# Kernel tuning notes

Hardware: AMD Instinct MI355X
Metric: run time of the kernel (lower is better)

The kernel has to match this reference:

```python
import jax, jax.numpy as jnp
import numpy as np

S = 3        # message passing steps
L = 128      # latent size
N = 10000    # nodes
E = 160000   # edges
DN, DE, DG = 64, 16, 8
OUT = 8
EPS = 1e-5


def _ln(x, scale, offset):
    m = jnp.mean(x, axis=-1, keepdims=True)
    v = jnp.var(x, axis=-1, keepdims=True)
    return (x - m) * jax.lax.rsqrt(v + EPS) * scale + offset


def _mlp(x, W0, b0, W1, b1):
    h = jax.nn.relu(x @ W0 + b0)
    return jax.nn.relu(h @ W1 + b1)


def setup_inputs() -> dict:
    key = jax.random.key(0)
    ks = iter(jax.random.split(key, 64))

    def w(shape, fan_in):
        return jax.random.normal(next(ks), shape, jnp.float32) / np.sqrt(fan_in).astype(np.float32)

    inp = {
        "nodes": jax.random.normal(next(ks), (N, DN), jnp.float32),
        "edges": jax.random.normal(next(ks), (E, DE), jnp.float32),
        "globals_": jax.random.normal(next(ks), (1, DG), jnp.float32),
        "senders": jax.random.randint(next(ks), (E,), 0, N),
        "receivers": jax.random.randint(next(ks), (E,), 0, N),
        # embedder
        "emb_node_W": w((DN, L), DN), "emb_node_b": jnp.zeros((L,), jnp.float32),
        "emb_edge_W": w((DE, L), DE), "emb_edge_b": jnp.zeros((L,), jnp.float32),
        "emb_glob_W": w((DG, L), DG), "emb_glob_b": jnp.zeros((L,), jnp.float32),
        # per-step MLPs (2 layers each)
        "edge_W0": w((S, 4 * L, L), 4 * L), "edge_b0": jnp.zeros((S, L), jnp.float32),
        "edge_W1": w((S, L, L), L),         "edge_b1": jnp.zeros((S, L), jnp.float32),
        "node_W0": w((S, 4 * L, L), 4 * L), "node_b0": jnp.zeros((S, L), jnp.float32),
        "node_W1": w((S, L, L), L),         "node_b1": jnp.zeros((S, L), jnp.float32),
        "glob_W0": w((S, 3 * L, L), 3 * L), "glob_b0": jnp.zeros((S, L), jnp.float32),
        "glob_W1": w((S, L, L), L),         "glob_b1": jnp.zeros((S, L), jnp.float32),
        # per-step layernorm (0: nodes, 1: edges, 2: globals)
        "ln_scale": jnp.ones((S, 3, L), jnp.float32),
        "ln_offset": jnp.zeros((S, 3, L), jnp.float32),
        # decoder (globals only)
        "dec_W": w((L, OUT), L), "dec_b": jnp.zeros((OUT,), jnp.float32),
    }
    return inp


def reference(nodes, edges, globals_, senders, receivers,
              emb_node_W, emb_node_b, emb_edge_W, emb_edge_b, emb_glob_W, emb_glob_b,
              edge_W0, edge_b0, edge_W1, edge_b1,
              node_W0, node_b0, node_W1, node_b1,
              glob_W0, glob_b0, glob_W1, glob_b1,
              ln_scale, ln_offset, dec_W, dec_b):
    # embed to latent
    n = nodes @ emb_node_W + emb_node_b      # [N, L]
    e = edges @ emb_edge_W + emb_edge_b      # [E, L]
    g = globals_ @ emb_glob_W + emb_glob_b   # [1, L]

    for s in range(S):
        # edge update: concat(edges, nodes[senders], nodes[receivers], globals)
        g_e = jnp.broadcast_to(g, (e.shape[0], L))
        e_in = jnp.concatenate([e, n[senders], n[receivers], g_e], axis=-1)  # [E, 4L]
        e_new = _mlp(e_in, edge_W0[s], edge_b0[s], edge_W1[s], edge_b1[s])
        # node update: concat(nodes, segsum(e,senders), segsum(e,receivers), globals)
        sent_agg = jax.ops.segment_sum(e_new, senders, num_segments=N)
        recv_agg = jax.ops.segment_sum(e_new, receivers, num_segments=N)
        g_n = jnp.broadcast_to(g, (N, L))
        n_in = jnp.concatenate([n, sent_agg, recv_agg, g_n], axis=-1)  # [N, 4L]
        n_new = _mlp(n_in, node_W0[s], node_b0[s], node_W1[s], node_b1[s])
        # global update: concat(node_agg, edge_agg, globals) (single graph)
        node_agg = jnp.sum(n_new, axis=0, keepdims=True)
        edge_agg = jnp.sum(e_new, axis=0, keepdims=True)
        g_in = jnp.concatenate([node_agg, edge_agg, g], axis=-1)  # [1, 3L]
        g_new = _mlp(g_in, glob_W0[s], glob_b0[s], glob_W1[s], glob_b1[s])
        # residual + layernorm
        n = _ln(n_new + n, ln_scale[s, 0], ln_offset[s, 0])
        e = _ln(e_new + e, ln_scale[s, 1], ln_offset[s, 1])
        g = _ln(g_new + g, ln_scale[s, 2], ln_offset[s, 2])

    # decoder maps globals only
    return g @ dec_W + dec_b  # [1, OUT]
```

## Files before the change

kernel.cpp:

```cpp
#include <hip/hip_runtime.h>
#include <hip/hip_bf16.h>

typedef __bf16 bf16;
typedef __bf16 bf16x8 __attribute__((ext_vector_type(8)));
typedef __bf16 bf16x4 __attribute__((ext_vector_type(4)));
typedef float  f32x4  __attribute__((ext_vector_type(4)));

#define NL 128
#define NN 10000
#define NE 160000
#define LN_EPS 1e-5f

__device__ __forceinline__ f32x4 f4zero() {
    f32x4 v; v[0] = 0.f; v[1] = 0.f; v[2] = 0.f; v[3] = 0.f; return v;
}

__device__ __forceinline__ int swz_off(int row, int b) {
    return row * 256 + (b ^ ((row & 7) << 4));
}

__device__ __forceinline__ bf16x8 frag_ld(const bf16* base, int row, int kbyte) {
    return *reinterpret_cast<const bf16x8*>(
        reinterpret_cast<const char*>(base) + swz_off(row, kbyte));
}

template <int NT>
__device__ __forceinline__ void stage_img(const bf16* __restrict__ img, bf16* dst, int tid) {
    #pragma unroll
    for (int i = 0; i < 2048 / NT; ++i) {
        int byte = (i * NT + tid) * 16;
        *reinterpret_cast<bf16x8*>(reinterpret_cast<char*>(dst) + byte) =
            *reinterpret_cast<const bf16x8*>(reinterpret_cast<const char*>(img) + byte);
    }
}

template <int NT>
__device__ __forceinline__ void stage_img_ld(const bf16* __restrict__ img, bf16x8* r, int tid) {
    #pragma unroll
    for (int i = 0; i < 2048 / NT; ++i)
        r[i] = *reinterpret_cast<const bf16x8*>(reinterpret_cast<const char*>(img) +
                                                (i * NT + tid) * 16);
}
template <int NT>
__device__ __forceinline__ void stage_img_st(bf16* dst, const bf16x8* r, int tid) {
    #pragma unroll
    for (int i = 0; i < 2048 / NT; ++i)
        *reinterpret_cast<bf16x8*>(reinterpret_cast<char*>(dst) + (i * NT + tid) * 16) = r[i];
}

__device__ __forceinline__ void stage_rows16(const float* __restrict__ src0, bf16* sX,
                                             int wrow0, int lane) {
    int c8 = (lane & 15) * 8;
    #pragma unroll
    for (int i = 0; i < 4; ++i) {
        int sub = i * 4 + (lane >> 4);
        const float* src = src0 + (size_t)sub * 128 + c8;
        f32x4 a = *reinterpret_cast<const f32x4*>(src);
        f32x4 b = *reinterpret_cast<const f32x4*>(src + 4);
        bf16x8 v;
        v[0] = (bf16)a[0]; v[1] = (bf16)a[1]; v[2] = (bf16)a[2]; v[3] = (bf16)a[3];
        v[4] = (bf16)b[0]; v[5] = (bf16)b[1]; v[6] = (bf16)b[2]; v[7] = (bf16)b[3];
        *reinterpret_cast<bf16x8*>(reinterpret_cast<char*>(sX) + swz_off(wrow0 + sub, c8 * 2)) = v;
    }
}

__device__ __forceinline__ void mfma_16x128(const bf16* sA, const bf16* sB, int arow, int kq,
                                            f32x4 acc[8]) {
    #pragma unroll
    for (int kk = 0; kk < 4; ++kk) {
        bf16x8 af = frag_ld(sA, arow, kk * 64 + kq);
        #pragma unroll
        for (int t = 0; t < 8; ++t) {
            bf16x8 bfr = frag_ld(sB, t * 16 + (arow & 15), kk * 64 + kq);
            acc[t] = __builtin_amdgcn_mfma_f32_16x16x32_bf16(af, bfr, acc[t], 0, 0, 0);
        }
    }
}

__device__ __forceinline__ void acc_to_lds_bf16(bf16* sX, const f32x4 acc[8], int w, int lane) {
    int c0 = lane & 15;
    #pragma unroll
    for (int r = 0; r < 4; ++r) {
        int rl = w * 16 + (lane >> 4) * 4 + r;
        #pragma unroll
        for (int t = 0; t < 8; ++t) {
            int col = t * 16 + c0;
            *reinterpret_cast<bf16*>(reinterpret_cast<char*>(sX) + swz_off(rl, col * 2)) =
                (bf16)acc[t][r];
        }
    }
}

__device__ __forceinline__ void lds_rows_to_global_bf16(const bf16* sX, bf16* __restrict__ dst0,
                                                        int w, int lane) {
    int c8 = (lane & 15) * 8;
    #pragma unroll
    for (int i = 0; i < 4; ++i) {
        int sub = i * 4 + (lane >> 4);
        bf16x8 v = *reinterpret_cast<const bf16x8*>(
            reinterpret_cast<const char*>(sX) + swz_off(w * 16 + sub, c8 * 2));
        *reinterpret_cast<bf16x8*>(dst0 + (size_t)sub * 128 + c8) = v;
    }
}

__global__ void k_prep(const float* __restrict__ eW0, const float* __restrict__ eW1,
                       const float* __restrict__ nW0, const float* __restrict__ nW1,
                       bf16* __restrict__ imgs, const float* __restrict__ globals_,
                       const float* __restrict__ embW, const float* __restrict__ embB,
                       float* __restrict__ g, const float* __restrict__ eb0,
                       const float* __restrict__ nb0, float* __restrict__ gve,
                       float* __restrict__ gvn, int* __restrict__ deg,
                       float* __restrict__ eagg, float* __restrict__ nagg,
                       int* __restrict__ done) {
    const int b = blockIdx.x;
    const int tid = threadIdx.x;
    if (b < 24) {
        const int s = b >> 3, kind = b & 7;
        const float* src;
        if (kind < 3)       src = eW0 + (size_t)s * 512 * 128 + (size_t)kind * 128 * 128;
        else if (kind == 3) src = eW1 + (size_t)s * 128 * 128;
        else if (kind < 7)  src = nW0 + (size_t)s * 512 * 128 + (size_t)(kind - 4) * 128 * 128;
        else                src = nW1 + (size_t)s * 128 * 128;
        bf16* img = imgs + (size_t)b * 16384;
        for (int i = 0; i < 16; ++i) {
            int q = tid + i * 256;
            int col = q & 127;
            int k0 = (q >> 7) << 2;
            bf16x4 v;
            v[0] = (bf16)src[(k0 + 0) * 128 + col];
            v[1] = (bf16)src[(k0 + 1) * 128 + col];
            v[2] = (bf16)src[(k0 + 2) * 128 + col];
            v[3] = (bf16)src[(k0 + 3) * 128 + col];
            *reinterpret_cast<bf16x4*>(reinterpret_cast<char*>(img) + swz_off(col, k0 * 2)) = v;
        }
    } else if (b == 24) {
        __shared__ float sG[128];
        if (tid < 3) done[tid] = 0;
        if (tid < 128) {
            float a = embB[tid];
            #pragma unroll
            for (int k = 0; k < 8; ++k) a += globals_[k] * embW[k * 128 + tid];
            g[tid] = a;
            sG[tid] = a;
        }
        __syncthreads();
        if (tid < 128) {
            const float* eW0g = eW0 + 384 * 128;
            const float* nW0g = nW0 + 384 * 128;
            float ae = eb0[tid], an = nb0[tid];
            for (int k = 0; k < 128; ++k) {
                float gv = sG[k];
                ae += gv * eW0g[k * 128 + tid];
                an += gv * nW0g[k * 128 + tid];
            }
            gve[tid] = ae;
            gvn[tid] = an;
        }
    } else {
        for (int i = tid; i < 2 * NN; i += 256) deg[i] = 0;
        for (int i = tid; i < 8 * 128; i += 256) eagg[i] = 0.f;
        for (int i = tid; i < 4 * 128; i += 256) nagg[i] = 0.f;
    }
}


__global__ void k_hist(const int* __restrict__ senders, const int* __restrict__ receivers,
                       int* __restrict__ deg_s, int* __restrict__ deg_r) {
    int i = blockIdx.x * 256 + threadIdx.x;
    if (i < NE) {
        atomicAdd(&deg_s[senders[i]], 1);
        atomicAdd(&deg_r[receivers[i]], 1);
    }
}

__device__ void scan_arr(const int* __restrict__ deg, int* __restrict__ rs, int* __restrict__ cur,
                         int* sW, int* sRun) {
    const int tid = threadIdx.x, lane = tid & 63, wid = tid >> 6;
    if (tid == 0) *sRun = 0;
    __syncthreads();
    for (int base = 0; base < NN; base += 1024) {
        int i = base + tid;
        int orig = (i < NN) ? deg[i] : 0;
        int v = orig;
        #pragma unroll
        for (int off = 1; off < 64; off <<= 1) {
            int u = __shfl_up(v, off, 64);
            if (lane >= off) v += u;
        }
        if (lane == 63) sW[wid] = v;
        __syncthreads();
        if (wid == 0 && lane < 16) {
            int u = sW[lane];
            #pragma unroll
            for (int off = 1; off < 16; off <<= 1) {
                int t = __shfl_up(u, off, 16);
                if (lane >= off) u += t;
            }
            sW[lane] = u;
        }
        __syncthreads();
        int waveoff = (wid == 0) ? 0 : sW[wid - 1];
        int incl = v + waveoff + *sRun;
        if (i < NN) {
            rs[i + 1] = incl;
            cur[i] = incl - orig;
        }
        __syncthreads();
        if (tid == 1023) *sRun = incl;
        __syncthreads();
    }
    if (tid == 0) rs[0] = 0;
}

__global__ void k_scan(const int* __restrict__ deg_s, int* __restrict__ rs_s,
                       int* __restrict__ cur_s, const int* __restrict__ deg_r,
                       int* __restrict__ rs_r, int* __restrict__ cur_r) {
    __shared__ int sW[16];
    __shared__ int sRun;
    scan_arr(deg_s, rs_s, cur_s, sW, &sRun);
    __syncthreads();
    scan_arr(deg_r, rs_r, cur_r, sW, &sRun);
}

__global__ void k_scatter_s(const int* __restrict__ senders, const int* __restrict__ receivers,
                            int* __restrict__ cur_s, int* __restrict__ perm,
                            int* __restrict__ snd_s, int* __restrict__ rcv_s) {
    int i = blockIdx.x * 256 + threadIdx.x;
    if (i < NE) {
        int s = senders[i];
        int p = atomicAdd(&cur_s[s], 1);
        perm[p] = i;
        snd_s[p] = s;
        rcv_s[p] = receivers[i];
    }
}

__global__ void k_scatter_r(const int* __restrict__ rcv_s, int* __restrict__ cur_r,
                            int* __restrict__ csr_r) {
    int j = blockIdx.x * 256 + threadIdx.x;
    if (j < NE) {
        int r = rcv_s[j];
        int p = atomicAdd(&cur_r[r], 1);
        csr_r[p] = j;
    }
}


__global__ __launch_bounds__(256, 2) void k_embed_nodes(
    const float* __restrict__ nodes, const float* __restrict__ W, const float* __restrict__ b,
    float* __restrict__ n_out, const bf16* __restrict__ imgPs, const bf16* __restrict__ imgPr,
    bf16* __restrict__ nsW, bf16* __restrict__ nrW) {
    __shared__ __align__(16) char smem[81920];
    float* sWemb = (float*)smem;
    float* sB = (float*)(smem + 32768);
    bf16* sWa = (bf16*)smem;
    bf16* sWb = (bf16*)(smem + 32768);
    bf16* sX = (bf16*)(smem + 65536);
    const int tid = threadIdx.x;
    const int lane = tid & 63;
    const int w = tid >> 6;
    const int rowbase = blockIdx.x * 64;
    const bool wvalid = (rowbase + w * 16) < NN;

    for (int i = tid; i < 64 * 128; i += 256) sWemb[i] = W[i];
    if (tid < 128) sB[tid] = b[tid];
    __syncthreads();

    const int rg = tid >> 4;
    const int c8 = (tid & 15) * 8;
    #pragma unroll
    for (int p = 0; p < 4; ++p) {
        int row = rowbase + p * 16 + rg;
        if (row < NN) {
            const f32x4* x4 = reinterpret_cast<const f32x4*>(nodes + (size_t)row * 64);
            float o[8];
            #pragma unroll
            for (int j = 0; j < 8; ++j) o[j] = sB[c8 + j];
            #pragma unroll
            for (int k4 = 0; k4 < 16; ++k4) {
                f32x4 xv = x4[k4];
                #pragma unroll
                for (int kk = 0; kk < 4; ++kk) {
                    float x = xv[kk];
                    const float* wrow = sWemb + (k4 * 4 + kk) * 128 + c8;
                    f32x4 wA = *reinterpret_cast<const f32x4*>(wrow);
                    f32x4 wB = *reinterpret_cast<const f32x4*>(wrow + 4);
                    o[0] += x * wA[0]; o[1] += x * wA[1]; o[2] += x * wA[2]; o[3] += x * wA[3];
                    o[4] += x * wB[0]; o[5] += x * wB[1]; o[6] += x * wB[2]; o[7] += x * wB[3];
                }
            }
            f32x4 oA, oB;
            bf16x8 v;
            #pragma unroll
            for (int j = 0; j < 8; ++j) {
                if (j < 4) oA[j] = o[j]; else oB[j - 4] = o[j];
                v[j] = (bf16)o[j];
            }
            float* orow = n_out + (size_t)row * 128 + c8;
            *reinterpret_cast<f32x4*>(orow) = oA;
            *reinterpret_cast<f32x4*>(orow + 4) = oB;
            *reinterpret_cast<bf16x8*>(reinterpret_cast<char*>(sX) +
                                       swz_off(p * 16 + rg, c8 * 2)) = v;
        }
    }
    __syncthreads();
    stage_img<256>(imgPs, sWa, tid);
    stage_img<256>(imgPr, sWb, tid);
    __syncthreads();
    if (!wvalid) return;

    const int arow = w * 16 + (lane & 15);
    const int kq = (lane >> 4) * 16;
    f32x4 acc[8], acc2[8];
    #pragma unroll
    for (int t = 0; t < 8; ++t) { acc[t] = f4zero(); acc2[t] = f4zero(); }
    mfma_16x128(sX, sWa, arow, kq, acc);
    mfma_16x128(sX, sWb, arow, kq, acc2);

    acc_to_lds_bf16(sX, acc, w, lane);
    lds_rows_to_global_bf16(sX, nsW + (size_t)(rowbase + w * 16) * 128, w, lane);
    acc_to_lds_bf16(sX, acc2, w, lane);
    lds_rows_to_global_bf16(sX, nrW + (size_t)(rowbase + w * 16) * 128, w, lane);
}

__global__ __launch_bounds__(256) void k_embed_edges(const float* __restrict__ edges,
                                                     const int* __restrict__ perm,
                                                     const float* __restrict__ W,
                                                     const float* __restrict__ b,
                                                     bf16* __restrict__ e_out) {
    __shared__ float sW[16 * 128];
    __shared__ float sB[128];
    const int tid = threadIdx.x;
    for (int i = tid; i < 16 * 128; i += 256) sW[i] = W[i];
    if (tid < 128) sB[tid] = b[tid];
    __syncthreads();
    const int rg = tid >> 4;
    const int c8 = (tid & 15) * 8;
    const int rowbase = blockIdx.x * 128;
    #pragma unroll 2
    for (int p = 0; p < 8; ++p) {
        int row = rowbase + p * 16 + rg;
        int src = perm[row];
        const f32x4* x4 = reinterpret_cast<const f32x4*>(edges + (size_t)src * 16);
        f32x4 xr0 = x4[0], xr1 = x4[1], xr2 = x4[2], xr3 = x4[3];
        float o[8];
        #pragma unroll
        for (int j = 0; j < 8; ++j) o[j] = sB[c8 + j];
        f32x4 xr[4] = {xr0, xr1, xr2, xr3};
        #pragma unroll
        for (int q = 0; q < 4; ++q) {
            #pragma unroll
            for (int kk = 0; kk < 4; ++kk) {
                float x = xr[q][kk];
                const float* wrow = sW + (q * 4 + kk) * 128 + c8;
                f32x4 wA = *reinterpret_cast<const f32x4*>(wrow);
                f32x4 wB = *reinterpret_cast<const f32x4*>(wrow + 4);
                o[0] += x * wA[0]; o[1] += x * wA[1]; o[2] += x * wA[2]; o[3] += x * wA[3];
                o[4] += x * wB[0]; o[5] += x * wB[1]; o[6] += x * wB[2]; o[7] += x * wB[3];
            }
        }
        bf16x8 v;
        #pragma unroll
        for (int j = 0; j < 8; ++j) v[j] = (bf16)o[j];
        *reinterpret_cast<bf16x8*>(e_out + (size_t)row * 128 + c8) = v;
    }
}


__global__ __launch_bounds__(512, 2) void k_edge(
    bf16* e_rw, bf16* __restrict__ e_new_out, const bf16* __restrict__ nsW,
    const bf16* __restrict__ nrW, float* __restrict__ edge_agg,
    const int* __restrict__ snd_s, const int* __restrict__ rcv_s,
    const bf16* __restrict__ imgW0, const bf16* __restrict__ imgW1,
    const float* __restrict__ gvec, const float* __restrict__ b1,
    const float* __restrict__ lnS, const float* __restrict__ lnO) {
    __shared__ __align__(16) char smem[65536];
    bf16* sW = (bf16*)smem;
    bf16* sX = (bf16*)(smem + 32768);
    float* sEagg = (float*)smem;

    const int tid = threadIdx.x;
    const int lane = tid & 63;
    const int w = tid >> 6;
    const int rowbase = blockIdx.x * 128;
    const int arow = w * 16 + (lane & 15);
    const int kq = (lane >> 4) * 16;
    const int c0 = lane & 15;
    const int qrt = lane >> 4;
    const int c8 = c0 * 8;

    stage_img<512>(imgW0, sW, tid);

    int snd_i[4], rcv_i[4];
    bf16x8 eold8[4];
    #pragma unroll
    for (int i = 0; i < 4; ++i) {
        int gr = rowbase + w * 16 + i * 4 + qrt;
        snd_i[i] = snd_s[gr];
        rcv_i[i] = rcv_s[gr];
        eold8[i] = *reinterpret_cast<const bf16x8*>(e_rw + (size_t)gr * 128 + c8);
    }

    f32x4 gvA = *reinterpret_cast<const f32x4*>(gvec + c8);
    f32x4 gvB = *reinterpret_cast<const f32x4*>(gvec + c8 + 4);
    f32x4 lsA = *reinterpret_cast<const f32x4*>(lnS + c8);
    f32x4 lsB = *reinterpret_cast<const f32x4*>(lnS + c8 + 4);
    f32x4 loA = *reinterpret_cast<const f32x4*>(lnO + c8);
    f32x4 loB = *reinterpret_cast<const f32x4*>(lnO + c8 + 4);
    float bb[8];
    #pragma unroll
    for (int t = 0; t < 8; ++t) bb[t] = b1[t * 16 + c0];

    bf16x8 ns8[4], nr8[4];
    #pragma unroll
    for (int i = 0; i < 4; ++i) {
        ns8[i] = *reinterpret_cast<const bf16x8*>(nsW + (size_t)snd_i[i] * 128 + c8);
        nr8[i] = *reinterpret_cast<const bf16x8*>(nrW + (size_t)rcv_i[i] * 128 + c8);
    }

    #pragma unroll
    for (int i = 0; i < 4; ++i)
        *reinterpret_cast<bf16x8*>(reinterpret_cast<char*>(sX) +
                                   swz_off(w * 16 + i * 4 + qrt, c8 * 2)) = eold8[i];

    __syncthreads();

    f32x4 acc[8];
    #pragma unroll
    for (int t = 0; t < 8; ++t) acc[t] = f4zero();
    __builtin_amdgcn_s_setprio(1);
    mfma_16x128(sX, sW, arow, kq, acc);
    __builtin_amdgcn_s_setprio(0);

    __syncthreads();

    bf16x8 w1r[4];
    stage_img_ld<512>(imgW1, w1r, tid);

    #pragma unroll
    for (int r = 0; r < 4; ++r) {
        int rl = w * 16 + (lane >> 4) * 4 + r;
        #pragma unroll
        for (int t = 0; t < 8; ++t)
            *reinterpret_cast<bf16*>(reinterpret_cast<char*>(sX) +
                                     swz_off(rl, (t * 16 + c0) * 2)) = (bf16)acc[t][r];
    }
    #pragma unroll
    for (int i = 0; i < 4; ++i) {
        int rl = w * 16 + i * 4 + qrt;
        bf16x8 a8 = *reinterpret_cast<const bf16x8*>(
            reinterpret_cast<const char*>(sX) + swz_off(rl, c8 * 2));
        bf16x8 h8;
        #pragma unroll
        for (int j = 0; j < 8; ++j) {
            float gvj = (j < 4) ? gvA[j] : gvB[j - 4];
            float v = (float)a8[j] + (float)ns8[i][j] + (float)nr8[i][j] + gvj;
            h8[j] = (bf16)fmaxf(v, 0.f);
        }
        *reinterpret_cast<bf16x8*>(reinterpret_cast<char*>(sX) + swz_off(rl, c8 * 2)) = h8;
    }

    stage_img_st<512>(sW, w1r, tid);
    __syncthreads();

    f32x4 acc2[8];
    #pragma unroll
    for (int t = 0; t < 8; ++t) acc2[t] = f4zero();
    __builtin_amdgcn_s_setprio(1);
    mfma_16x128(sX, sW, arow, kq, acc2);
    __builtin_amdgcn_s_setprio(0);

    #pragma unroll
    for (int r = 0; r < 4; ++r) {
        int rl = w * 16 + (lane >> 4) * 4 + r;
        #pragma unroll
        for (int t = 0; t < 8; ++t)
            *reinterpret_cast<bf16*>(reinterpret_cast<char*>(sX) +
                                     swz_off(rl, (t * 16 + c0) * 2)) =
                (bf16)fmaxf(acc2[t][r] + bb[t], 0.f);
    }

    float cs[8];
    #pragma unroll
    for (int j = 0; j < 8; ++j) cs[j] = 0.f;
    bf16* enew0 = e_new_out + (size_t)rowbase * 128;
    bf16* e0 = e_rw + (size_t)rowbase * 128;
    #pragma unroll
    for (int i = 0; i < 4; ++i) {
        int sub = w * 16 + i * 4 + qrt;
        bf16x8 en8 = *reinterpret_cast<const bf16x8*>(
            reinterpret_cast<const char*>(sX) + swz_off(sub, c8 * 2));
        *reinterpret_cast<bf16x8*>(enew0 + (size_t)sub * 128 + c8) = en8;
        float rv[8], s1 = 0.f, s2 = 0.f;
        #pragma unroll
        for (int j = 0; j < 8; ++j) {
            float en = (float)en8[j];
            cs[j] += en;
            float v = en + (float)eold8[i][j];
            rv[j] = v;
            s1 += v;
            s2 += v * v;
        }
        #pragma unroll
        for (int off = 1; off < 16; off <<= 1) {
            s1 += __shfl_xor(s1, off, 16);
            s2 += __shfl_xor(s2, off, 16);
        }
        float mean = s1 * (1.f / 128.f);
        float rstd = rsqrtf(s2 * (1.f / 128.f) - mean * mean + LN_EPS);
        bf16x8 o8;
        #pragma unroll
        for (int j = 0; j < 8; ++j) {
            float ls = (j < 4) ? lsA[j] : lsB[j - 4];
            float lo = (j < 4) ? loA[j] : loB[j - 4];
            o8[j] = (bf16)((rv[j] - mean) * rstd * ls + lo);
        }
        *reinterpret_cast<bf16x8*>(e0 + (size_t)sub * 128 + c8) = o8;
    }

    #pragma unroll
    for (int j = 0; j < 8; ++j) {
        cs[j] += __shfl_xor(cs[j], 16, 64);
        cs[j] += __shfl_xor(cs[j], 32, 64);
    }
    __syncthreads();
    if (qrt == 0) {
        float* dst = sEagg + w * 128 + c8;
        #pragma unroll
        for (int j = 0; j < 8; ++j) dst[j] = cs[j];
    }
    __syncthreads();
    if (tid < 128) {
        float v = 0.f;
        #pragma unroll
        for (int ww = 0; ww < 8; ++ww) v += sEagg[ww * 128 + tid];
        atomicAdd(&edge_agg[(blockIdx.x & 7) * 128 + tid], v);
    }
}

__global__ __launch_bounds__(256) void k_agg(const bf16* __restrict__ e_new,
                                             const int* __restrict__ rs_s,
                                             const int* __restrict__ rs_r,
                                             const int* __restrict__ csr_r,
                                             bf16* __restrict__ sent, bf16* __restrict__ recv) {
    const int lane = threadIdx.x & 63;
    const int w = threadIdx.x >> 6;
    const int node = blockIdx.x * 4 + w;
    if (node >= NN) return;
    const int qrt = lane >> 4;
    const int c8 = (lane & 15) * 8;
    float a[8];
    #pragma unroll
    for (int j = 0; j < 8; ++j) a[j] = 0.f;
    const int b0 = rs_s[node], b1 = rs_s[node + 1];
    for (int jj = b0 + qrt; jj < b1; jj += 4) {
        bf16x8 v = *reinterpret_cast<const bf16x8*>(e_new + (size_t)jj * 128 + c8);
        #pragma unroll
        for (int j = 0; j < 8; ++j) a[j] += (float)v[j];
    }
    #pragma unroll
    for (int j = 0; j < 8; ++j) {
        a[j] += __shfl_xor(a[j], 16, 64);
        a[j] += __shfl_xor(a[j], 32, 64);
    }
    if (qrt == 0) {
        bf16x8 o;
        #pragma unroll
        for (int j = 0; j < 8; ++j) o[j] = (bf16)a[j];
        *reinterpret_cast<bf16x8*>(sent + (size_t)node * 128 + c8) = o;
    }
    #pragma unroll
    for (int j = 0; j < 8; ++j) a[j] = 0.f;
    const int c1 = rs_r[node], c2 = rs_r[node + 1];
    for (int pp = c1 + qrt; pp < c2; pp += 4) {
        int jj = csr_r[pp];
        bf16x8 v = *reinterpret_cast<const bf16x8*>(e_new + (size_t)jj * 128 + c8);
        #pragma unroll
        for (int j = 0; j < 8; ++j) a[j] += (float)v[j];
    }
    #pragma unroll
    for (int j = 0; j < 8; ++j) {
        a[j] += __shfl_xor(a[j], 16, 64);
        a[j] += __shfl_xor(a[j], 32, 64);
    }
    if (qrt == 0) {
        bf16x8 o;
        #pragma unroll
        for (int j = 0; j < 8; ++j) o[j] = (bf16)a[j];
        *reinterpret_cast<bf16x8*>(recv + (size_t)node * 128 + c8) = o;
    }
}

__global__ __launch_bounds__(256, 2) void k_node(
    float* n_rw, const bf16* __restrict__ sent, const bf16* __restrict__ recv,
    float* __restrict__ node_agg , const bf16* __restrict__ imgW0,
    const bf16* __restrict__ imgW1, const float* __restrict__ gvec,
    const float* __restrict__ b1, const float* __restrict__ lnS,
    const float* __restrict__ lnO, const bf16* __restrict__ imgPs,
    const bf16* __restrict__ imgPr, bf16* __restrict__ nsW, bf16* __restrict__ nrW,
    int do_proj,
    int* __restrict__ done_ctr, float* __restrict__ edge_agg , float* __restrict__ g,
    const float* __restrict__ gW0, const float* __restrict__ gb0,
    const float* __restrict__ gW1, const float* __restrict__ gb1,
    const float* __restrict__ glnS, const float* __restrict__ glnO,
    const float* __restrict__ eW0g, const float* __restrict__ eb0n,
    const float* __restrict__ nW0g, const float* __restrict__ nb0n,
    float* __restrict__ gve, float* __restrict__ gvn, const float* __restrict__ decW,
    const float* __restrict__ decb, float* __restrict__ out, int do_next, int do_dec) {
    __shared__ __align__(16) char smem[81920];
    __shared__ int sLast;
    bf16* sA = (bf16*)smem;
    bf16* sB = (bf16*)(smem + 32768);
    bf16* sX = (bf16*)(smem + 65536);
    float* sNagg = (float*)smem;

    const int tid = threadIdx.x;
    const int lane = tid & 63;
    const int w = tid >> 6;
    const int rowbase = blockIdx.x * 64;
    const bool wvalid = (rowbase + w * 16) < NN;
    const int arow = w * 16 + (lane & 15);
    const int kq = (lane >> 4) * 16;
    const int c0 = lane & 15;
    const int qrt = lane >> 4;
    const int c8 = c0 * 8;

    stage_img<256>(imgW0, sA, tid);
    stage_img<256>(imgW0 + 16384, sB, tid);
    bf16x8 sent8[4], recv8[4];
    if (wvalid) {
        stage_rows16(n_rw + (size_t)(rowbase + w * 16) * 128, sX, w * 16, lane);
        #pragma unroll
        for (int i = 0; i < 4; ++i) {
            int gr = rowbase + w * 16 + i * 4 + qrt;
            sent8[i] = *reinterpret_cast<const bf16x8*>(sent + (size_t)gr * 128 + c8);
            recv8[i] = *reinterpret_cast<const bf16x8*>(recv + (size_t)gr * 128 + c8);
        }
    }
    __syncthreads();

    float gvf[8], bbf[8];
    #pragma unroll
    for (int t = 0; t < 8; ++t) {
        gvf[t] = gvec[t * 16 + c0];
        bbf[t] = b1[t * 16 + c0];
    }
    f32x4 lsA4 = *reinterpret_cast<const f32x4*>(lnS + c8);
    f32x4 lsB4 = *reinterpret_cast<const f32x4*>(lnS + c8 + 4);
    f32x4 loA4 = *reinterpret_cast<const f32x4*>(lnO + c8);
    f32x4 loB4 = *reinterpret_cast<const f32x4*>(lnO + c8 + 4);

    f32x4 acc[8];
    #pragma unroll
    for (int t = 0; t < 8; ++t) acc[t] = f4zero();
    float cs[8];
    #pragma unroll
    for (int j = 0; j < 8; ++j) cs[j] = 0.f;

    if (wvalid) mfma_16x128(sX, sA, arow, kq, acc);
    __syncthreads();

    stage_img<256>(imgW0 + 32768, sA, tid);
    if (wvalid) {
        #pragma unroll
        for (int i = 0; i < 4; ++i)
            *reinterpret_cast<bf16x8*>(reinterpret_cast<char*>(sX) +
                                       swz_off(w * 16 + i * 4 + qrt, c8 * 2)) = sent8[i];
        mfma_16x128(sX, sB, arow, kq, acc);
    }
    __syncthreads();

    stage_img<256>(imgW1, sB, tid);
    if (wvalid) {
        #pragma unroll
        for (int i = 0; i < 4; ++i)
            *reinterpret_cast<bf16x8*>(reinterpret_cast<char*>(sX) +
                                       swz_off(w * 16 + i * 4 + qrt, c8 * 2)) = recv8[i];
        mfma_16x128(sX, sA, arow, kq, acc);

        #pragma unroll
        for (int r = 0; r < 4; ++r) {
            int rl = w * 16 + (lane >> 4) * 4 + r;
            #pragma unroll
            for (int t = 0; t < 8; ++t)
                *reinterpret_cast<bf16*>(reinterpret_cast<char*>(sX) +
                                         swz_off(rl, (t * 16 + c0) * 2)) =
                    (bf16)fmaxf(acc[t][r] + gvf[t], 0.f);
        }
    }
    __syncthreads();

    if (wvalid) {
        #pragma unroll
        for (int t = 0; t < 8; ++t) acc[t] = f4zero();
        mfma_16x128(sX, sB, arow, kq, acc);
        #pragma unroll
        for (int r = 0; r < 4; ++r) {
            int rl = w * 16 + (lane >> 4) * 4 + r;
            #pragma unroll
            for (int t = 0; t < 8; ++t)
                *reinterpret_cast<bf16*>(reinterpret_cast<char*>(sX) +
                                         swz_off(rl, (t * 16 + c0) * 2)) =
                    (bf16)fmaxf(acc[t][r] + bbf[t], 0.f);
        }

        const float* nbase = n_rw + (size_t)(rowbase + w * 16) * 128;
        #pragma unroll
        for (int i = 0; i < 4; ++i) {
            int sub = i * 4 + qrt;
            bf16x8 en8 = *reinterpret_cast<const bf16x8*>(
                reinterpret_cast<const char*>(sX) + swz_off(w * 16 + sub, c8 * 2));
            f32x4 noA = *reinterpret_cast<const f32x4*>(nbase + (size_t)sub * 128 + c8);
            f32x4 noB = *reinterpret_cast<const f32x4*>(nbase + (size_t)sub * 128 + c8 + 4);
            float rv[8], s1 = 0.f, s2 = 0.f;
            #pragma unroll
            for (int j = 0; j < 8; ++j) {
                float en = (float)en8[j];
                cs[j] += en;
                float v = en + ((j < 4) ? noA[j] : noB[j - 4]);
                rv[j] = v;
                s1 += v;
                s2 += v * v;
            }
            #pragma unroll
            for (int off = 1; off < 16; off <<= 1) {
                s1 += __shfl_xor(s1, off, 16);
                s2 += __shfl_xor(s2, off, 16);
            }
            float mean = s1 * (1.f / 128.f);
            float rstd = rsqrtf(s2 * (1.f / 128.f) - mean * mean + LN_EPS);
            f32x4 oA, oB;
            bf16x8 l8;
            #pragma unroll
            for (int j = 0; j < 8; ++j) {
                float ls = (j < 4) ? lsA4[j] : lsB4[j - 4];
                float lo = (j < 4) ? loA4[j] : loB4[j - 4];
                float o = (rv[j] - mean) * rstd * ls + lo;
                if (j < 4) oA[j] = o; else oB[j - 4] = o;
                l8[j] = (bf16)o;
            }
            float* orow = n_rw + (size_t)(rowbase + w * 16 + sub) * 128 + c8;
            *reinterpret_cast<f32x4*>(orow) = oA;
            *reinterpret_cast<f32x4*>(orow + 4) = oB;
            *reinterpret_cast<bf16x8*>(reinterpret_cast<char*>(sX) +
                                       swz_off(w * 16 + sub, c8 * 2)) = l8;
        }
    }

    if (do_proj) {
        __syncthreads();
        stage_img<256>(imgPs, sA, tid);
        stage_img<256>(imgPr, sB, tid);
        __syncthreads();
        if (wvalid) {
            f32x4 pa[8], pb[8];
            #pragma unroll
            for (int t = 0; t < 8; ++t) { pa[t] = f4zero(); pb[t] = f4zero(); }
            mfma_16x128(sX, sA, arow, kq, pa);
            mfma_16x128(sX, sB, arow, kq, pb);
            acc_to_lds_bf16(sX, pa, w, lane);
            lds_rows_to_global_bf16(sX, nsW + (size_t)(rowbase + w * 16) * 128, w, lane);
            acc_to_lds_bf16(sX, pb, w, lane);
            lds_rows_to_global_bf16(sX, nrW + (size_t)(rowbase + w * 16) * 128, w, lane);
        }
    }

    #pragma unroll
    for (int j = 0; j < 8; ++j) {
        cs[j] += __shfl_xor(cs[j], 16, 64);
        cs[j] += __shfl_xor(cs[j], 32, 64);
    }
    __syncthreads();
    if (qrt == 0) {
        float* dst = sNagg + w * 128 + c8;
        #pragma unroll
        for (int j = 0; j < 8; ++j) dst[j] = wvalid ? cs[j] : 0.f;
    }
    __syncthreads();
    if (tid < 128) {
        float v = sNagg[tid] + sNagg[128 + tid] + sNagg[256 + tid] + sNagg[384 + tid];
        atomicAdd(&node_agg[(blockIdx.x & 3) * 128 + tid], v);
    }

    __syncthreads();
    if (tid == 0) {
        __threadfence();
        int old = atomicAdd(done_ctr, 1);
        sLast = (old == (int)gridDim.x - 1);
    }
    __syncthreads();
    if (!sLast) return;

    float* sIn = (float*)smem;
    float* sP0 = sIn + 384;
    float* sP1 = sP0 + 128;
    float* sH = sP1 + 128;
    float* sG = sH + 128;
    float* sMR = sG + 128;
    const int j = tid & 127;
    const int part = tid >> 7;

    if (tid < 128) {
        float v = 0.f;
        #pragma unroll
        for (int c = 0; c < 4; ++c) v += atomicAdd(&node_agg[c * 128 + tid], 0.f);
        #pragma unroll
        for (int c = 0; c < 4; ++c) atomicExch(&node_agg[c * 128 + tid], 0.f);
        sIn[tid] = v;
        sIn[256 + tid] = g[tid];
    } else {
        float v = 0.f;
        #pragma unroll
        for (int c = 0; c < 8; ++c) v += edge_agg[c * 128 + j];
        #pragma unroll
        for (int c = 0; c < 8; ++c) edge_agg[c * 128 + j] = 0.f;
        sIn[128 + j] = v;
    }
    __syncthreads();
    {
        float p = 0.f;
        for (int k = 0; k < 192; ++k) {
            int kk = part * 192 + k;
            p += sIn[kk] * gW0[(size_t)kk * 128 + j];
        }
        (part ? sP1 : sP0)[j] = p;
    }
    __syncthreads();
    if (tid < 128) sH[tid] = fmaxf(gb0[tid] + sP0[tid] + sP1[tid], 0.f);
    __syncthreads();
    {
        float p = 0.f;
        for (int k = 0; k < 64; ++k) {
            int kk = part * 64 + k;
            p += sH[kk] * gW1[(size_t)kk * 128 + j];
        }
        (part ? sP1 : sP0)[j] = p;
    }
    __syncthreads();
    float res = 0.f;
    if (tid < 128) {
        res = fmaxf(gb1[tid] + sP0[tid] + sP1[tid], 0.f) + sIn[256 + tid];
        sP0[tid] = res;
        sP1[tid] = res * res;
    }
    __syncthreads();
    if (tid < 64) {
        float a = sP0[tid] + sP0[tid + 64];
        float q = sP1[tid] + sP1[tid + 64];
        #pragma unroll
        for (int off = 1; off < 64; off <<= 1) {
            a += __shfl_xor(a, off, 64);
            q += __shfl_xor(q, off, 64);
        }
        if (tid == 0) {
            float m = a * (1.f / 128.f);
            float v = q * (1.f / 128.f) - m * m;
            sMR[0] = m;
            sMR[1] = rsqrtf(v + LN_EPS);
        }
    }
    __syncthreads();
    if (tid < 128) {
        float go = (res - sMR[0]) * sMR[1] * glnS[tid] + glnO[tid];
        g[tid] = go;
        sG[tid] = go;
    }
    __syncthreads();
    if (do_next) {
        float pe = 0.f, pn = 0.f;
        for (int k = 0; k < 64; ++k) {
            int kk = part * 64 + k;
            float gv = sG[kk];
            pe += gv * eW0g[(size_t)kk * 128 + j];
            pn += gv * nW0g[(size_t)kk * 128 + j];
        }
        (part ? sP1 : sP0)[j] = pe;
        sIn[part * 128 + j] = pn;
        __syncthreads();
        if (tid < 128) {
            gve[tid] = eb0n[tid] + sP0[tid] + sP1[tid];
            gvn[tid] = nb0n[tid] + sIn[tid] + sIn[128 + tid];
        }
    }
    if (do_dec && tid < 8) {
        float a = decb[tid];
        for (int k = 0; k < 128; ++k) a += sG[k] * decW[k * 8 + tid];
        out[tid] = a;
    }
}

extern "C" void kernel_launch(void* const* d_in, const int* in_sizes, int n_in, void* d_out,
                              int out_size, void* d_ws, size_t ws_size, hipStream_t stream) {
    (void)in_sizes; (void)n_in; (void)out_size; (void)ws_size;
    const float* nodes = (const float*)d_in[0];
    const float* edges = (const float*)d_in[1];
    const float* globals_ = (const float*)d_in[2];
    const int* senders = (const int*)d_in[3];
    const int* receivers = (const int*)d_in[4];
    const float* emb_node_W = (const float*)d_in[5];
    const float* emb_node_b = (const float*)d_in[6];
    const float* emb_edge_W = (const float*)d_in[7];
    const float* emb_edge_b = (const float*)d_in[8];
    const float* emb_glob_W = (const float*)d_in[9];
    const float* emb_glob_b = (const float*)d_in[10];
    const float* edge_W0 = (const float*)d_in[11];
    const float* edge_b0 = (const float*)d_in[12];
    const float* edge_W1 = (const float*)d_in[13];
    const float* edge_b1 = (const float*)d_in[14];
    const float* node_W0 = (const float*)d_in[15];
    const float* node_b0 = (const float*)d_in[16];
    const float* node_W1 = (const float*)d_in[17];
    const float* node_b1 = (const float*)d_in[18];
    const float* glob_W0 = (const float*)d_in[19];
    const float* glob_b0 = (const float*)d_in[20];
    const float* glob_W1 = (const float*)d_in[21];
    const float* glob_b1 = (const float*)d_in[22];
    const float* ln_scale = (const float*)d_in[23];
    const float* ln_offset = (const float*)d_in[24];
    const float* dec_W = (const float*)d_in[25];
    const float* dec_b = (const float*)d_in[26];

    char* ws = (char*)d_ws;
    size_t off = 0;
    auto alloc = [&](size_t bytes) -> char* {
        char* p = ws + off;
        off += (bytes + 255) & ~(size_t)255;
        return p;
    };
    bf16* e = (bf16*)alloc((size_t)NE * NL * 2);
    bf16* e_new = (bf16*)alloc((size_t)NE * NL * 2);
    float* n = (float*)alloc((size_t)NN * NL * 4);
    bf16* nsW = (bf16*)alloc((size_t)NN * NL * 2);
    bf16* nrW = (bf16*)alloc((size_t)NN * NL * 2);
    bf16* sent = (bf16*)alloc((size_t)NN * NL * 2);
    bf16* recv = (bf16*)alloc((size_t)NN * NL * 2);
    bf16* imgs = (bf16*)alloc((size_t)24 * 16384 * 2);
    float* eagg = (float*)alloc(8 * 128 * 4);
    float* nagg = (float*)alloc(4 * 128 * 4);
    float* g = (float*)alloc(128 * 4);
    float* gve = (float*)alloc(128 * 4);
    float* gvn = (float*)alloc(128 * 4);
    int* done = (int*)alloc(16 * 4);
    int* deg = (int*)alloc((size_t)2 * NN * 4);
    int* deg_s = deg;
    int* deg_r = deg + NN;
    int* rs_s = (int*)alloc((size_t)(NN + 1) * 4);
    int* rs_r = (int*)alloc((size_t)(NN + 1) * 4);
    int* cur_s = (int*)alloc((size_t)NN * 4);
    int* cur_r = (int*)alloc((size_t)NN * 4);
    int* perm = (int*)alloc((size_t)NE * 4);
    int* snd_s = (int*)alloc((size_t)NE * 4);
    int* rcv_s = (int*)alloc((size_t)NE * 4);
    int* csr_r = (int*)alloc((size_t)NE * 4);

    const int NB_N = (NN + 63) / 64;
    const int NB_E = NE / 128;
    const int NB_EMB = NE / 128;
    const int NB_SC = (NE + 255) / 256;
    const int NB_AGG = NN / 4;

    auto img = [&](int s, int kind) -> const bf16* {
        return imgs + ((size_t)s * 8 + kind) * 16384;
    };

    k_prep<<<26, 256, 0, stream>>>(edge_W0, edge_W1, node_W0, node_W1, imgs, globals_,
                                   emb_glob_W, emb_glob_b, g, edge_b0, node_b0, gve, gvn,
                                   deg, eagg, nagg, done);

    k_hist<<<NB_SC, 256, 0, stream>>>(senders, receivers, deg_s, deg_r);
    k_scan<<<1, 1024, 0, stream>>>(deg_s, rs_s, cur_s, deg_r, rs_r, cur_r);
    k_scatter_s<<<NB_SC, 256, 0, stream>>>(senders, receivers, cur_s, perm, snd_s, rcv_s);
    k_scatter_r<<<NB_SC, 256, 0, stream>>>(rcv_s, cur_r, csr_r);

    k_embed_nodes<<<NB_N, 256, 0, stream>>>(nodes, emb_node_W, emb_node_b, n, img(0, 1),
                                            img(0, 2), nsW, nrW);
    k_embed_edges<<<NB_EMB, 256, 0, stream>>>(edges, perm, emb_edge_W, emb_edge_b, e);

    for (int s = 0; s < 3; ++s) {
        const int last = (s == 2);
        k_edge<<<NB_E, 512, 0, stream>>>(e, e_new, nsW, nrW, eagg, snd_s, rcv_s, img(s, 0),
                                         img(s, 3), gve, edge_b1 + s * 128,
                                         ln_scale + (s * 3 + 1) * 128,
                                         ln_offset + (s * 3 + 1) * 128);
        k_agg<<<NB_AGG, 256, 0, stream>>>(e_new, rs_s, rs_r, csr_r, sent, recv);
        const float* eW0g = last ? edge_W0 : edge_W0 + (size_t)(s + 1) * 512 * 128 + 384 * 128;
        const float* eb0n = last ? edge_b0 : edge_b0 + (s + 1) * 128;
        const float* nW0g = last ? node_W0 : node_W0 + (size_t)(s + 1) * 512 * 128 + 384 * 128;
        const float* nb0n = last ? node_b0 : node_b0 + (s + 1) * 128;
        k_node<<<NB_N, 256, 0, stream>>>(
            n, sent, recv, nagg, img(s, 4), img(s, 7), gvn, node_b1 + s * 128,
            ln_scale + (s * 3 + 0) * 128, ln_offset + (s * 3 + 0) * 128,
            img(last ? 0 : s + 1, 1), img(last ? 0 : s + 1, 2), nsW, nrW, !last,
            done + s, eagg, g, glob_W0 + (size_t)s * 384 * 128, glob_b0 + s * 128,
            glob_W1 + (size_t)s * 128 * 128, glob_b1 + s * 128, ln_scale + (s * 3 + 2) * 128,
            ln_offset + (s * 3 + 2) * 128, eW0g, eb0n, nW0g, nb0n, gve, gvn, dec_W, dec_b,
            (float*)d_out, !last, last);
    }
}
```

Measured before the change: 401.0 us.

## Read MFMA weight fragments from global, fuse sender aggregation into edge kernel

Weight images are pre-laid out in per-lane MFMA fragment order so the GEMMs load B fragments straight from global or L2 instead of staging them into LDS. Shared memory drops sharply and most block barriers go away, and the edge kernel now runs 64-row, 256-thread blocks to raise occupancy. Sender-side segment sums move into the edge kernel as run-length fp32 atomics, using the fact that edges are sorted by sender. The fp32 sent buffer is zeroed in the prep kernel and re-zeroed by the node kernel after it is read. This trades LDS reuse for repeated global fragment reads and adds atomic traffic.

```diff
diff --git a/kernel.cpp b/kernel.cpp
--- a/kernel.cpp
+++ b/kernel.cpp
@@ -3,11 +3,11 @@
 
 typedef __bf16 bf16;
 typedef __bf16 bf16x8 __attribute__((ext_vector_type(8)));
-typedef __bf16 bf16x4 __attribute__((ext_vector_type(4)));
 typedef float  f32x4  __attribute__((ext_vector_type(4)));
 
 #define NL 128
 #define NN 10000
+#define NNPAD 10048
 #define NE 160000
 #define LN_EPS 1e-5f
 
@@ -22,30 +22,6 @@
 __device__ __forceinline__ bf16x8 frag_ld(const bf16* base, int row, int kbyte) {
     return *reinterpret_cast<const bf16x8*>(
         reinterpret_cast<const char*>(base) + swz_off(row, kbyte));
-}
-
-template <int NT>
-__device__ __forceinline__ void stage_img(const bf16* __restrict__ img, bf16* dst, int tid) {
-    #pragma unroll
-    for (int i = 0; i < 2048 / NT; ++i) {
-        int byte = (i * NT + tid) * 16;
-        *reinterpret_cast<bf16x8*>(reinterpret_cast<char*>(dst) + byte) =
-            *reinterpret_cast<const bf16x8*>(reinterpret_cast<const char*>(img) + byte);
-    }
-}
-
-template <int NT>
-__device__ __forceinline__ void stage_img_ld(const bf16* __restrict__ img, bf16x8* r, int tid) {
-    #pragma unroll
-    for (int i = 0; i < 2048 / NT; ++i)
-        r[i] = *reinterpret_cast<const bf16x8*>(reinterpret_cast<const char*>(img) +
-                                                (i * NT + tid) * 16);
-}
-template <int NT>
-__device__ __forceinline__ void stage_img_st(bf16* dst, const bf16x8* r, int tid) {
-    #pragma unroll
-    for (int i = 0; i < 2048 / NT; ++i)
-        *reinterpret_cast<bf16x8*>(reinterpret_cast<char*>(dst) + (i * NT + tid) * 16) = r[i];
 }
 
 __device__ __forceinline__ void stage_rows16(const float* __restrict__ src0, bf16* sX,
@@ -64,14 +40,15 @@
     }
 }
 
-__device__ __forceinline__ void mfma_16x128(const bf16* sA, const bf16* sB, int arow, int kq,
-                                            f32x4 acc[8]) {
+__device__ __forceinline__ void mfma_16x128g(const bf16* sA, const bf16* __restrict__ imgB,
+                                             int arow, int kq, int lane, f32x4 acc[8]) {
     #pragma unroll
     for (int kk = 0; kk < 4; ++kk) {
         bf16x8 af = frag_ld(sA, arow, kk * 64 + kq);
         #pragma unroll
         for (int t = 0; t < 8; ++t) {
-            bf16x8 bfr = frag_ld(sB, t * 16 + (arow & 15), kk * 64 + kq);
+            bf16x8 bfr = *reinterpret_cast<const bf16x8*>(
+                imgB + (size_t)(((kk * 8 + t) * 64 + lane)) * 8);
             acc[t] = __builtin_amdgcn_mfma_f32_16x16x32_bf16(af, bfr, acc[t], 0, 0, 0);
         }
     }
@@ -111,7 +88,7 @@
                        const float* __restrict__ nb0, float* __restrict__ gve,
                        float* __restrict__ gvn, int* __restrict__ deg,
                        float* __restrict__ eagg, float* __restrict__ nagg,
-                       int* __restrict__ done) {
+                       float* __restrict__ sent, int* __restrict__ done) {
     const int b = blockIdx.x;
     const int tid = threadIdx.x;
     if (b < 24) {
@@ -122,16 +99,18 @@
         else if (kind < 7)  src = nW0 + (size_t)s * 512 * 128 + (size_t)(kind - 4) * 128 * 128;
         else                src = nW1 + (size_t)s * 128 * 128;
         bf16* img = imgs + (size_t)b * 16384;
-        for (int i = 0; i < 16; ++i) {
+        #pragma unroll
+        for (int i = 0; i < 8; ++i) {
             int q = tid + i * 256;
-            int col = q & 127;
-            int k0 = (q >> 7) << 2;
-            bf16x4 v;
-            v[0] = (bf16)src[(k0 + 0) * 128 + col];
-            v[1] = (bf16)src[(k0 + 1) * 128 + col];
-            v[2] = (bf16)src[(k0 + 2) * 128 + col];
-            v[3] = (bf16)src[(k0 + 3) * 128 + col];
-            *reinterpret_cast<bf16x4*>(reinterpret_cast<char*>(img) + swz_off(col, k0 * 2)) = v;
+            int l = q & 63;
+            int ft = q >> 6;
+            int kk = ft >> 3, t = ft & 7;
+            int col = t * 16 + (l & 15);
+            int k0 = kk * 32 + (l >> 4) * 8;
+            bf16x8 v;
+            #pragma unroll
+            for (int j = 0; j < 8; ++j) v[j] = (bf16)src[(size_t)(k0 + j) * 128 + col];
+            *reinterpret_cast<bf16x8*>(img + (size_t)q * 8) = v;
         }
     } else if (b == 24) {
         __shared__ float sG[128];
@@ -156,10 +135,17 @@
             gve[tid] = ae;
             gvn[tid] = an;
         }
-    } else {
+    } else if (b == 25) {
         for (int i = tid; i < 2 * NN; i += 256) deg[i] = 0;
         for (int i = tid; i < 8 * 128; i += 256) eagg[i] = 0.f;
         for (int i = tid; i < 4 * 128; i += 256) nagg[i] = 0.f;
+    } else {
+        const int chunk = NNPAD * 128 / 16;
+        float* base = sent + (size_t)(b - 26) * chunk;
+        for (int i = tid * 4; i < chunk; i += 1024) {
+            f32x4 z = f4zero();
+            *reinterpret_cast<f32x4*>(base + i) = z;
+        }
     }
 }
 
@@ -250,12 +236,10 @@
     const float* __restrict__ nodes, const float* __restrict__ W, const float* __restrict__ b,
     float* __restrict__ n_out, const bf16* __restrict__ imgPs, const bf16* __restrict__ imgPr,
     bf16* __restrict__ nsW, bf16* __restrict__ nrW) {
-    __shared__ __align__(16) char smem[81920];
+    __shared__ __align__(16) char smem[49664];
     float* sWemb = (float*)smem;
     float* sB = (float*)(smem + 32768);
-    bf16* sWa = (bf16*)smem;
-    bf16* sWb = (bf16*)(smem + 32768);
-    bf16* sX = (bf16*)(smem + 65536);
+    bf16* sX = (bf16*)(smem + 33280);
     const int tid = threadIdx.x;
     const int lane = tid & 63;
     const int w = tid >> 6;
@@ -267,7 +251,7 @@
     __syncthreads();
 
     const int rg = tid >> 4;
-    const int c8 = (tid & 15) * 8;
+    const int c8e = (tid & 15) * 8;
     #pragma unroll
     for (int p = 0; p < 4; ++p) {
         int row = rowbase + p * 16 + rg;
@@ -275,14 +259,14 @@
             const f32x4* x4 = reinterpret_cast<const f32x4*>(nodes + (size_t)row * 64);
             float o[8];
             #pragma unroll
-            for (int j = 0; j < 8; ++j) o[j] = sB[c8 + j];
+            for (int j = 0; j < 8; ++j) o[j] = sB[c8e + j];
             #pragma unroll
             for (int k4 = 0; k4 < 16; ++k4) {
                 f32x4 xv = x4[k4];
                 #pragma unroll
                 for (int kk = 0; kk < 4; ++kk) {
                     float x = xv[kk];
-                    const float* wrow = sWemb + (k4 * 4 + kk) * 128 + c8;
+                    const float* wrow = sWemb + (k4 * 4 + kk) * 128 + c8e;
                     f32x4 wA = *reinterpret_cast<const f32x4*>(wrow);
                     f32x4 wB = *reinterpret_cast<const f32x4*>(wrow + 4);
                     o[0] += x * wA[0]; o[1] += x * wA[1]; o[2] += x * wA[2]; o[3] += x * wA[3];
@@ -296,16 +280,13 @@
                 if (j < 4) oA[j] = o[j]; else oB[j - 4] = o[j];
                 v[j] = (bf16)o[j];
             }
-            float* orow = n_out + (size_t)row * 128 + c8;
+            float* orow = n_out + (size_t)row * 128 + c8e;
             *reinterpret_cast<f32x4*>(orow) = oA;
             *reinterpret_cast<f32x4*>(orow + 4) = oB;
             *reinterpret_cast<bf16x8*>(reinterpret_cast<char*>(sX) +
-                                       swz_off(p * 16 + rg, c8 * 2)) = v;
-        }
-    }
-    __syncthreads();
-    stage_img<256>(imgPs, sWa, tid);
-    stage_img<256>(imgPr, sWb, tid);
+                                       swz_off(p * 16 + rg, c8e * 2)) = v;
+        }
+    }
     __syncthreads();
     if (!wvalid) return;
 
@@ -314,8 +295,8 @@
     f32x4 acc[8], acc2[8];
     #pragma unroll
     for (int t = 0; t < 8; ++t) { acc[t] = f4zero(); acc2[t] = f4zero(); }
-    mfma_16x128(sX, sWa, arow, kq, acc);
-    mfma_16x128(sX, sWb, arow, kq, acc2);
+    mfma_16x128g(sX, imgPs, arow, kq, lane, acc);
+    mfma_16x128g(sX, imgPr, arow, kq, lane, acc2);
 
     acc_to_lds_bf16(sX, acc, w, lane);
     lds_rows_to_global_bf16(sX, nsW + (size_t)(rowbase + w * 16) * 128, w, lane);
@@ -342,11 +323,10 @@
         int row = rowbase + p * 16 + rg;
         int src = perm[row];
         const f32x4* x4 = reinterpret_cast<const f32x4*>(edges + (size_t)src * 16);
-        f32x4 xr0 = x4[0], xr1 = x4[1], xr2 = x4[2], xr3 = x4[3];
+        f32x4 xr[4] = {x4[0], x4[1], x4[2], x4[3]};
         float o[8];
         #pragma unroll
         for (int j = 0; j < 8; ++j) o[j] = sB[c8 + j];
-        f32x4 xr[4] = {xr0, xr1, xr2, xr3};
         #pragma unroll
         for (int q = 0; q < 4; ++q) {
             #pragma unroll
@@ -367,112 +347,98 @@
 }
 
 
-__global__ __launch_bounds__(512, 2) void k_edge(
+__global__ __launch_bounds__(256) void k_edge(
     bf16* e_rw, bf16* __restrict__ e_new_out, const bf16* __restrict__ nsW,
-    const bf16* __restrict__ nrW, float* __restrict__ edge_agg,
+    const bf16* __restrict__ nrW, float* __restrict__ sent, float* __restrict__ edge_agg,
     const int* __restrict__ snd_s, const int* __restrict__ rcv_s,
     const bf16* __restrict__ imgW0, const bf16* __restrict__ imgW1,
     const float* __restrict__ gvec, const float* __restrict__ b1,
     const float* __restrict__ lnS, const float* __restrict__ lnO) {
-    __shared__ __align__(16) char smem[65536];
-    bf16* sW = (bf16*)smem;
-    bf16* sX = (bf16*)(smem + 32768);
-    float* sEagg = (float*)smem;
+    __shared__ __align__(16) char smem[18432];
+    bf16* sX = (bf16*)smem;
+    float* sEagg = (float*)(smem + 16384);
 
     const int tid = threadIdx.x;
     const int lane = tid & 63;
     const int w = tid >> 6;
-    const int rowbase = blockIdx.x * 128;
+    const int rowbase = blockIdx.x * 64;
     const int arow = w * 16 + (lane & 15);
     const int kq = (lane >> 4) * 16;
     const int c0 = lane & 15;
     const int qrt = lane >> 4;
     const int c8 = c0 * 8;
 
-    stage_img<512>(imgW0, sW, tid);
-
     int snd_i[4], rcv_i[4];
     bf16x8 eold8[4];
     #pragma unroll
     for (int i = 0; i < 4; ++i) {
-        int gr = rowbase + w * 16 + i * 4 + qrt;
+        int gr = rowbase + w * 16 + qrt * 4 + i;
         snd_i[i] = snd_s[gr];
         rcv_i[i] = rcv_s[gr];
         eold8[i] = *reinterpret_cast<const bf16x8*>(e_rw + (size_t)gr * 128 + c8);
     }
-
+    bf16x8 ns8[4], nr8[4];
+    #pragma unroll
+    for (int i = 0; i < 4; ++i) {
+        ns8[i] = *reinterpret_cast<const bf16x8*>(nsW + (size_t)snd_i[i] * 128 + c8);
+        nr8[i] = *reinterpret_cast<const bf16x8*>(nrW + (size_t)rcv_i[i] * 128 + c8);
+    }
     f32x4 gvA = *reinterpret_cast<const f32x4*>(gvec + c8);
     f32x4 gvB = *reinterpret_cast<const f32x4*>(gvec + c8 + 4);
+
+    #pragma unroll
+    for (int i = 0; i < 4; ++i)
+        *reinterpret_cast<bf16x8*>(reinterpret_cast<char*>(sX) +
+                                   swz_off(w * 16 + qrt * 4 + i, c8 * 2)) = eold8[i];
+
+    f32x4 acc[8];
+    #pragma unroll
+    for (int t = 0; t < 8; ++t) acc[t] = f4zero();
+    __builtin_amdgcn_s_setprio(1);
+    mfma_16x128g(sX, imgW0, arow, kq, lane, acc);
+    __builtin_amdgcn_s_setprio(0);
+
+    #pragma unroll
+    for (int r = 0; r < 4; ++r) {
+        int rl = w * 16 + qrt * 4 + r;
+        #pragma unroll
+        for (int t = 0; t < 8; ++t)
+            *reinterpret_cast<bf16*>(reinterpret_cast<char*>(sX) +
+                                     swz_off(rl, (t * 16 + c0) * 2)) = (bf16)acc[t][r];
+    }
+    #pragma unroll
+    for (int i = 0; i < 4; ++i) {
+        int rl = w * 16 + qrt * 4 + i;
+        bf16x8 a8 = *reinterpret_cast<const bf16x8*>(
+            reinterpret_cast<const char*>(sX) + swz_off(rl, c8 * 2));
+        bf16x8 h8;
+        #pragma unroll
+        for (int j = 0; j < 8; ++j) {
+            float gvj = (j < 4) ? gvA[j] : gvB[j - 4];
+            float v = (float)a8[j] + (float)ns8[i][j] + (float)nr8[i][j] + gvj;
+            h8[j] = (bf16)fmaxf(v, 0.f);
+        }
+        *reinterpret_cast<bf16x8*>(reinterpret_cast<char*>(sX) + swz_off(rl, c8 * 2)) = h8;
+    }
+
+    f32x4 acc2[8];
+    #pragma unroll
+    for (int t = 0; t < 8; ++t) acc2[t] = f4zero();
+    __builtin_amdgcn_s_setprio(1);
+    mfma_16x128g(sX, imgW1, arow, kq, lane, acc2);
+    __builtin_amdgcn_s_setprio(0);
+
+    float bb[8];
+    #pragma unroll
+    for (int t = 0; t < 8; ++t) bb[t] = b1[t * 16 + c0];
     f32x4 lsA = *reinterpret_cast<const f32x4*>(lnS + c8);
     f32x4 lsB = *reinterpret_cast<const f32x4*>(lnS + c8 + 4);
     f32x4 loA = *reinterpret_cast<const f32x4*>(lnO + c8);
     f32x4 loB = *reinterpret_cast<const f32x4*>(lnO + c8 + 4);
-    float bb[8];
-    #pragma unroll
-    for (int t = 0; t < 8; ++t) bb[t] = b1[t * 16 + c0];
-
-    bf16x8 ns8[4], nr8[4];
-    #pragma unroll
-    for (int i = 0; i < 4; ++i) {
-        ns8[i] = *reinterpret_cast<const bf16x8*>(nsW + (size_t)snd_i[i] * 128 + c8);
-        nr8[i] = *reinterpret_cast<const bf16x8*>(nrW + (size_t)rcv_i[i] * 128 + c8);
-    }
-
-    #pragma unroll
-    for (int i = 0; i < 4; ++i)
-        *reinterpret_cast<bf16x8*>(reinterpret_cast<char*>(sX) +
-                                   swz_off(w * 16 + i * 4 + qrt, c8 * 2)) = eold8[i];
-
-    __syncthreads();
-
-    f32x4 acc[8];
-    #pragma unroll
-    for (int t = 0; t < 8; ++t) acc[t] = f4zero();
-    __builtin_amdgcn_s_setprio(1);
-    mfma_16x128(sX, sW, arow, kq, acc);
-    __builtin_amdgcn_s_setprio(0);
-
-    __syncthreads();
-
-    bf16x8 w1r[4];
-    stage_img_ld<512>(imgW1, w1r, tid);
 
     #pragma unroll
     for (int r = 0; r < 4; ++r) {
-        int rl = w * 16 + (lane >> 4) * 4 + r;
-        #pragma unroll
-        for (int t = 0; t < 8; ++t)
-            *reinterpret_cast<bf16*>(reinterpret_cast<char*>(sX) +
-                                     swz_off(rl, (t * 16 + c0) * 2)) = (bf16)acc[t][r];
-    }
-    #pragma unroll
-    for (int i = 0; i < 4; ++i) {
-        int rl = w * 16 + i * 4 + qrt;
-        bf16x8 a8 = *reinterpret_cast<const bf16x8*>(
-            reinterpret_cast<const char*>(sX) + swz_off(rl, c8 * 2));
-        bf16x8 h8;
-        #pragma unroll
-        for (int j = 0; j < 8; ++j) {
-            float gvj = (j < 4) ? gvA[j] : gvB[j - 4];
-            float v = (float)a8[j] + (float)ns8[i][j] + (float)nr8[i][j] + gvj;
-            h8[j] = (bf16)fmaxf(v, 0.f);
-        }
-        *reinterpret_cast<bf16x8*>(reinterpret_cast<char*>(sX) + swz_off(rl, c8 * 2)) = h8;
-    }
-
-    stage_img_st<512>(sW, w1r, tid);
-    __syncthreads();
-
-    f32x4 acc2[8];
-    #pragma unroll
-    for (int t = 0; t < 8; ++t) acc2[t] = f4zero();
-    __builtin_amdgcn_s_setprio(1);
-    mfma_16x128(sX, sW, arow, kq, acc2);
-    __builtin_amdgcn_s_setprio(0);
-
-    #pragma unroll
-    for (int r = 0; r < 4; ++r) {
-        int rl = w * 16 + (lane >> 4) * 4 + r;
+        int rl = w * 16 + qrt * 4 + r;
         #pragma unroll
         for (int t = 0; t < 8; ++t)
             *reinterpret_cast<bf16*>(reinterpret_cast<char*>(sX) +
@@ -480,22 +446,32 @@
                 (bf16)fmaxf(acc2[t][r] + bb[t], 0.f);
     }
 
-    float cs[8];
-    #pragma unroll
-    for (int j = 0; j < 8; ++j) cs[j] = 0.f;
+    float cs[8], run[8];
+    #pragma unroll
+    for (int j = 0; j < 8; ++j) { cs[j] = 0.f; run[j] = 0.f; }
+    int curn = snd_i[0];
     bf16* enew0 = e_new_out + (size_t)rowbase * 128;
     bf16* e0 = e_rw + (size_t)rowbase * 128;
     #pragma unroll
     for (int i = 0; i < 4; ++i) {
-        int sub = w * 16 + i * 4 + qrt;
+        int sub = w * 16 + qrt * 4 + i;
         bf16x8 en8 = *reinterpret_cast<const bf16x8*>(
             reinterpret_cast<const char*>(sX) + swz_off(sub, c8 * 2));
         *reinterpret_cast<bf16x8*>(enew0 + (size_t)sub * 128 + c8) = en8;
+        if (snd_i[i] != curn) {
+            #pragma unroll
+            for (int j = 0; j < 8; ++j) {
+                atomicAdd(&sent[(size_t)curn * 128 + c8 + j], run[j]);
+                run[j] = 0.f;
+            }
+            curn = snd_i[i];
+        }
         float rv[8], s1 = 0.f, s2 = 0.f;
         #pragma unroll
         for (int j = 0; j < 8; ++j) {
             float en = (float)en8[j];
             cs[j] += en;
+            run[j] += en;
             float v = en + (float)eold8[i][j];
             rv[j] = v;
             s1 += v;
@@ -517,6 +493,9 @@
         }
         *reinterpret_cast<bf16x8*>(e0 + (size_t)sub * 128 + c8) = o8;
     }
+    #pragma unroll
+    for (int j = 0; j < 8; ++j)
+        atomicAdd(&sent[(size_t)curn * 128 + c8 + j], run[j]);
 
     #pragma unroll
     for (int j = 0; j < 8; ++j) {
@@ -531,18 +510,15 @@
     }
     __syncthreads();
     if (tid < 128) {
-        float v = 0.f;
-        #pragma unroll
-        for (int ww = 0; ww < 8; ++ww) v += sEagg[ww * 128 + tid];
+        float v = sEagg[tid] + sEagg[128 + tid] + sEagg[256 + tid] + sEagg[384 + tid];
         atomicAdd(&edge_agg[(blockIdx.x & 7) * 128 + tid], v);
     }
 }
 
 __global__ __launch_bounds__(256) void k_agg(const bf16* __restrict__ e_new,
-                                             const int* __restrict__ rs_s,
                                              const int* __restrict__ rs_r,
                                              const int* __restrict__ csr_r,
-                                             bf16* __restrict__ sent, bf16* __restrict__ recv) {
+                                             bf16* __restrict__ recv) {
     const int lane = threadIdx.x & 63;
     const int w = threadIdx.x >> 6;
     const int node = blockIdx.x * 4 + w;
@@ -552,25 +528,6 @@
     float a[8];
     #pragma unroll
     for (int j = 0; j < 8; ++j) a[j] = 0.f;
-    const int b0 = rs_s[node], b1 = rs_s[node + 1];
-    for (int jj = b0 + qrt; jj < b1; jj += 4) {
-        bf16x8 v = *reinterpret_cast<const bf16x8*>(e_new + (size_t)jj * 128 + c8);
-        #pragma unroll
-        for (int j = 0; j < 8; ++j) a[j] += (float)v[j];
-    }
-    #pragma unroll
-    for (int j = 0; j < 8; ++j) {
-        a[j] += __shfl_xor(a[j], 16, 64);
-        a[j] += __shfl_xor(a[j], 32, 64);
-    }
-    if (qrt == 0) {
-        bf16x8 o;
-        #pragma unroll
-        for (int j = 0; j < 8; ++j) o[j] = (bf16)a[j];
-        *reinterpret_cast<bf16x8*>(sent + (size_t)node * 128 + c8) = o;
-    }
-    #pragma unroll
-    for (int j = 0; j < 8; ++j) a[j] = 0.f;
     const int c1 = rs_r[node], c2 = rs_r[node + 1];
     for (int pp = c1 + qrt; pp < c2; pp += 4) {
         int jj = csr_r[pp];
@@ -591,8 +548,8 @@
     }
 }
 
-__global__ __launch_bounds__(256, 2) void k_node(
-    float* n_rw, const bf16* __restrict__ sent, const bf16* __restrict__ recv,
+__global__ __launch_bounds__(256) void k_node(
+    float* n_rw, float* __restrict__ sent, const bf16* __restrict__ recv,
     float* __restrict__ node_agg , const bf16* __restrict__ imgW0,
     const bf16* __restrict__ imgW1, const float* __restrict__ gvec,
     const float* __restrict__ b1, const float* __restrict__ lnS,
@@ -607,12 +564,10 @@
     const float* __restrict__ nW0g, const float* __restrict__ nb0n,
     float* __restrict__ gve, float* __restrict__ gvn, const float* __restrict__ decW,
     const float* __restrict__ decb, float* __restrict__ out, int do_next, int do_dec) {
-    __shared__ __align__(16) char smem[81920];
+    __shared__ __align__(16) char smem[18432];
     __shared__ int sLast;
-    bf16* sA = (bf16*)smem;
-    bf16* sB = (bf16*)(smem + 32768);
-    bf16* sX = (bf16*)(smem + 65536);
-    float* sNagg = (float*)smem;
+    bf16* sX = (bf16*)smem;
+    float* sNagg = (float*)(smem + 16384);
 
     const int tid = threadIdx.x;
     const int lane = tid & 63;
@@ -625,19 +580,33 @@
     const int qrt = lane >> 4;
     const int c8 = c0 * 8;
 
-    stage_img<256>(imgW0, sA, tid);
-    stage_img<256>(imgW0 + 16384, sB, tid);
-    bf16x8 sent8[4], recv8[4];
+    f32x4 stA[4], stB[4];
+    bf16x8 recv8[4];
     if (wvalid) {
-        stage_rows16(n_rw + (size_t)(rowbase + w * 16) * 128, sX, w * 16, lane);
         #pragma unroll
         for (int i = 0; i < 4; ++i) {
             int gr = rowbase + w * 16 + i * 4 + qrt;
-            sent8[i] = *reinterpret_cast<const bf16x8*>(sent + (size_t)gr * 128 + c8);
+            const float* sp = sent + (size_t)gr * 128 + c8;
+            stA[i] = *reinterpret_cast<const f32x4*>(sp);
+            stB[i] = *reinterpret_cast<const f32x4*>(sp + 4);
             recv8[i] = *reinterpret_cast<const bf16x8*>(recv + (size_t)gr * 128 + c8);
         }
-    }
-    __syncthreads();
+        stage_rows16(n_rw + (size_t)(rowbase + w * 16) * 128, sX, w * 16, lane);
+    }
+    bf16x8 sent8[4];
+    #pragma unroll
+    for (int i = 0; i < 4; ++i) {
+        #pragma unroll
+        for (int j = 0; j < 8; ++j)
+            sent8[i][j] = (bf16)((j < 4) ? stA[i][j] : stB[i][j - 4]);
+    }
+
+    f32x4 acc[8];
+    #pragma unroll
+    for (int t = 0; t < 8; ++t) acc[t] = f4zero();
+    float cs[8];
+    #pragma unroll
+    for (int j = 0; j < 8; ++j) cs[j] = 0.f;
 
     float gvf[8], bbf[8];
     #pragma unroll
@@ -650,53 +619,35 @@
     f32x4 loA4 = *reinterpret_cast<const f32x4*>(lnO + c8);
     f32x4 loB4 = *reinterpret_cast<const f32x4*>(lnO + c8 + 4);
 
-    f32x4 acc[8];
-    #pragma unroll
-    for (int t = 0; t < 8; ++t) acc[t] = f4zero();
-    float cs[8];
-    #pragma unroll
-    for (int j = 0; j < 8; ++j) cs[j] = 0.f;
-
-    if (wvalid) mfma_16x128(sX, sA, arow, kq, acc);
-    __syncthreads();
-
-    stage_img<256>(imgW0 + 32768, sA, tid);
     if (wvalid) {
+        mfma_16x128g(sX, imgW0, arow, kq, lane, acc);
         #pragma unroll
         for (int i = 0; i < 4; ++i)
             *reinterpret_cast<bf16x8*>(reinterpret_cast<char*>(sX) +
                                        swz_off(w * 16 + i * 4 + qrt, c8 * 2)) = sent8[i];
-        mfma_16x128(sX, sB, arow, kq, acc);
-    }
-    __syncthreads();
-
-    stage_img<256>(imgW1, sB, tid);
-    if (wvalid) {
+        mfma_16x128g(sX, imgW0 + 16384, arow, kq, lane, acc);
         #pragma unroll
         for (int i = 0; i < 4; ++i)
             *reinterpret_cast<bf16x8*>(reinterpret_cast<char*>(sX) +
                                        swz_off(w * 16 + i * 4 + qrt, c8 * 2)) = recv8[i];
-        mfma_16x128(sX, sA, arow, kq, acc);
+        mfma_16x128g(sX, imgW0 + 32768, arow, kq, lane, acc);
 
         #pragma unroll
         for (int r = 0; r < 4; ++r) {
-            int rl = w * 16 + (lane >> 4) * 4 + r;
+            int rl = w * 16 + qrt * 4 + r;
             #pragma unroll
             for (int t = 0; t < 8; ++t)
                 *reinterpret_cast<bf16*>(reinterpret_cast<char*>(sX) +
                                          swz_off(rl, (t * 16 + c0) * 2)) =
                     (bf16)fmaxf(acc[t][r] + gvf[t], 0.f);
         }
-    }
-    __syncthreads();
-
-    if (wvalid) {
+
         #pragma unroll
         for (int t = 0; t < 8; ++t) acc[t] = f4zero();
-        mfma_16x128(sX, sB, arow, kq, acc);
+        mfma_16x128g(sX, imgW1, arow, kq, lane, acc);
         #pragma unroll
         for (int r = 0; r < 4; ++r) {
-            int rl = w * 16 + (lane >> 4) * 4 + r;
+            int rl = w * 16 + qrt * 4 + r;
             #pragma unroll
             for (int t = 0; t < 8; ++t)
                 *reinterpret_cast<bf16*>(reinterpret_cast<char*>(sX) +
@@ -745,24 +696,26 @@
             *reinterpret_cast<bf16x8*>(reinterpret_cast<char*>(sX) +
                                        swz_off(w * 16 + sub, c8 * 2)) = l8;
         }
-    }
-
-    if (do_proj) {
-        __syncthreads();
-        stage_img<256>(imgPs, sA, tid);
-        stage_img<256>(imgPr, sB, tid);
-        __syncthreads();
-        if (wvalid) {
+
+        if (do_proj) {
             f32x4 pa[8], pb[8];
             #pragma unroll
             for (int t = 0; t < 8; ++t) { pa[t] = f4zero(); pb[t] = f4zero(); }
-            mfma_16x128(sX, sA, arow, kq, pa);
-            mfma_16x128(sX, sB, arow, kq, pb);
+            mfma_16x128g(sX, imgPs, arow, kq, lane, pa);
+            mfma_16x128g(sX, imgPr, arow, kq, lane, pb);
             acc_to_lds_bf16(sX, pa, w, lane);
             lds_rows_to_global_bf16(sX, nsW + (size_t)(rowbase + w * 16) * 128, w, lane);
             acc_to_lds_bf16(sX, pb, w, lane);
             lds_rows_to_global_bf16(sX, nrW + (size_t)(rowbase + w * 16) * 128, w, lane);
         }
+    }
+
+    {
+        float* sb = sent + (size_t)rowbase * 128;
+        f32x4 z = f4zero();
+        #pragma unroll
+        for (int ii = 0; ii < 8; ++ii)
+            *reinterpret_cast<f32x4*>(sb + ii * 1024 + tid * 4) = z;
     }
 
     #pragma unroll
@@ -932,7 +885,7 @@
     float* n = (float*)alloc((size_t)NN * NL * 4);
     bf16* nsW = (bf16*)alloc((size_t)NN * NL * 2);
     bf16* nrW = (bf16*)alloc((size_t)NN * NL * 2);
-    bf16* sent = (bf16*)alloc((size_t)NN * NL * 2);
+    float* sent = (float*)alloc((size_t)NNPAD * NL * 4);
     bf16* recv = (bf16*)alloc((size_t)NN * NL * 2);
     bf16* imgs = (bf16*)alloc((size_t)24 * 16384 * 2);
     float* eagg = (float*)alloc(8 * 128 * 4);
@@ -954,7 +907,7 @@
     int* csr_r = (int*)alloc((size_t)NE * 4);
 
     const int NB_N = (NN + 63) / 64;
-    const int NB_E = NE / 128;
+    const int NB_E = NE / 64;
     const int NB_EMB = NE / 128;
     const int NB_SC = (NE + 255) / 256;
     const int NB_AGG = NN / 4;
@@ -963,9 +916,9 @@
         return imgs + ((size_t)s * 8 + kind) * 16384;
     };
 
-    k_prep<<<26, 256, 0, stream>>>(edge_W0, edge_W1, node_W0, node_W1, imgs, globals_,
+    k_prep<<<42, 256, 0, stream>>>(edge_W0, edge_W1, node_W0, node_W1, imgs, globals_,
                                    emb_glob_W, emb_glob_b, g, edge_b0, node_b0, gve, gvn,
-                                   deg, eagg, nagg, done);
+                                   deg, eagg, nagg, sent, done);
 
     k_hist<<<NB_SC, 256, 0, stream>>>(senders, receivers, deg_s, deg_r);
     k_scan<<<1, 1024, 0, stream>>>(deg_s, rs_s, cur_s, deg_r, rs_r, cur_r);
@@ -978,11 +931,11 @@
 
     for (int s = 0; s < 3; ++s) {
         const int last = (s == 2);
-        k_edge<<<NB_E, 512, 0, stream>>>(e, e_new, nsW, nrW, eagg, snd_s, rcv_s, img(s, 0),
-                                         img(s, 3), gve, edge_b1 + s * 128,
+        k_edge<<<NB_E, 256, 0, stream>>>(e, e_new, nsW, nrW, sent, eagg, snd_s, rcv_s,
+                                         img(s, 0), img(s, 3), gve, edge_b1 + s * 128,
                                          ln_scale + (s * 3 + 1) * 128,
                                          ln_offset + (s * 3 + 1) * 128);
-        k_agg<<<NB_AGG, 256, 0, stream>>>(e_new, rs_s, rs_r, csr_r, sent, recv);
+        k_agg<<<NB_AGG, 256, 0, stream>>>(e_new, rs_r, csr_r, recv);
         const float* eW0g = last ? edge_W0 : edge_W0 + (size_t)(s + 1) * 512 * 128 + 384 * 128;
         const float* eb0n = last ? edge_b0 : edge_b0 + (s + 1) * 128;
         const float* nW0g = last ? node_W0 : node_W0 + (size_t)(s + 1) * 512 * 128 + 384 * 128;
```

Result: slower. 957.1 us (+138.7%).
